# Kernel tuning notes

Measured on AMD Instinct MI355X. Metric: run time of the kernel, lower is better.

Reference implementation:

```python
import jax, jax.numpy as jnp
import numpy as np

S = 512      # num_seg (queries)
T = 16384    # frames
D = 512      # d_model
DFF = 2048   # dim_feedforward
EPS = 1e-5


def layer_norm(x, g, b):
    mu = jnp.mean(x, axis=-1, keepdims=True)
    var = jnp.mean((x - mu) ** 2, axis=-1, keepdims=True)
    return (x - mu) * jax.lax.rsqrt(var + EPS) * g + b


def setup_inputs() -> dict:
    key = jax.random.key(0)
    ks = jax.random.split(key, 16)
    inv = 1.0 / np.sqrt(D)
    invf = 1.0 / np.sqrt(DFF)
    # action_idx: exactly S contiguous segments over T frames
    action_idx = (jnp.arange(T, dtype=jnp.int32) * S) // T
    return {
        "tgt": jax.random.normal(ks[0], (S, 1, D), jnp.float32),
        "memory": jax.random.normal(ks[1], (T, 1, D), jnp.float32),
        "pos": jax.random.normal(ks[2], (T, 1, D), jnp.float32),
        "query_pos": jax.random.normal(ks[3], (S, 1, D), jnp.float32),
        "action_idx": action_idx,
        "W_tgt2": jax.random.uniform(ks[4], (D, D), jnp.float32, -inv, inv),
        "b_tgt2": jax.random.uniform(ks[5], (D,), jnp.float32, -inv, inv),
        "W1": jax.random.uniform(ks[6], (DFF, D), jnp.float32, -inv, inv),
        "b1": jax.random.uniform(ks[7], (DFF,), jnp.float32, -inv, inv),
        "W2": jax.random.uniform(ks[8], (D, DFF), jnp.float32, -invf, invf),
        "b2": jax.random.uniform(ks[9], (D,), jnp.float32, -invf, invf),
        "g2": jnp.ones((D,), jnp.float32),
        "be2": jnp.zeros((D,), jnp.float32),
        "g3": jnp.ones((D,), jnp.float32),
        "be3": jnp.zeros((D,), jnp.float32),
    }


def reference(tgt, memory, pos, query_pos, action_idx,
              W_tgt2, b_tgt2, W1, b1, W2, b2, g2, be2, g3, be3):
    num_seg, _, dim = tgt.shape
    q = tgt + query_pos          # [S, 1, D]
    k = memory + pos             # [T, 1, D]
    v = memory                   # [T, 1, D]

    # segment-neighbor mask: seg_id per frame; query s attends to frames in
    # segments {s-1, s, s+1}
    change = jnp.concatenate([jnp.zeros((1,), jnp.int32),
                              (action_idx[1:] != action_idx[:-1]).astype(jnp.int32)])
    seg_id = jnp.cumsum(change)                                   # [T]
    mask = jnp.abs(seg_id[None, :] - jnp.arange(num_seg)[:, None]) <= 1  # [S, T]

    scores = jnp.einsum("sbd,tbd->bst", q, k) / np.sqrt(dim)      # [1, S, T]
    scores = jnp.where(mask[None], scores, -jnp.inf)
    attn = jax.nn.softmax(scores, axis=-1)                        # [1, S, T]

    ctx = jnp.einsum("bst,tbd->sbd", attn, v)                     # [S, 1, D]
    tgt2 = jax.nn.relu(ctx) @ W_tgt2.T + b_tgt2                   # [S, 1, D]
    x = layer_norm(tgt + tgt2, g2, be2)
    ffn = jax.nn.relu(x @ W1.T + b1) @ W2.T + b2
    out = layer_norm(x + ffn, g3, be3)
    return out
```

## Files before the change

### kernel.cpp

```cpp
#include <hip/hip_runtime.h>
#include <math.h>

#define S_Q  512
#define T_F  16384
#define D_M  512
#define DFF_ 2048
#define SEG  32
#define SCALE 0.04419417382415922f

typedef __attribute__((ext_vector_type(8))) short short8;
typedef __attribute__((ext_vector_type(4))) float floatx4;

__device__ __forceinline__ unsigned short f2bf(float f) {
    unsigned int u = __builtin_bit_cast(unsigned int, f);
    u += 0x7FFFu + ((u >> 16) & 1u);
    return (unsigned short)(u >> 16);
}

__device__ __forceinline__ void async_copy16(const void* g, void* l) {
    __builtin_amdgcn_global_load_lds(
        (const __attribute__((address_space(1))) void*)g,
        (__attribute__((address_space(3))) void*)l, 16, 0, 0);
}

__global__ __launch_bounds__(256) void conv3_bf16(
    const float* __restrict__ w0, unsigned short* __restrict__ o0, int n0,
    const float* __restrict__ w1, unsigned short* __restrict__ o1, int n1,
    const float* __restrict__ w2, unsigned short* __restrict__ o2)
{
    int i = (blockIdx.x * 256 + threadIdx.x) * 4;
    const float* src; unsigned short* dst;
    if (i < n0)            { src = w0; dst = o0; }
    else if (i < n0 + n1)  { src = w1; dst = o1; i -= n0; }
    else                   { src = w2; dst = o2; i -= n0 + n1; }
    const float4 v = *(const float4*)(src + i);
    unsigned short o[4] = {f2bf(v.x), f2bf(v.y), f2bf(v.z), f2bf(v.w)};
    *(uint2*)(dst + i) = *(const uint2*)o;
}

__global__ __launch_bounds__(256) void attn_seg(
    const float* __restrict__ tgt, const float* __restrict__ memory,
    const float* __restrict__ pos, const float* __restrict__ qp,
    float* __restrict__ part,
    float2* __restrict__ me)
{
    const int j    = blockIdx.x;
    const int tid  = threadIdx.x;
    const int lane = tid & 63;
    const int wave = tid >> 6;

    __shared__ float v[SEG * D_M];
    __shared__ float sc[3][SEG];
    __shared__ float pr[3][SEG];

    {
        const float* g = memory + (size_t)j * SEG * D_M + (size_t)wave * 16 * 256 + lane * 4;
        #pragma unroll
        for (int r = 0; r < 16; ++r)
            async_copy16(g + r * 256, v + (wave * 16 + r) * 256);
    }

    float q0[8] = {}, q1[8] = {}, q2[8] = {};
    {
        const int d = lane * 8;
        if (j > 0) {
            const float4 a0 = *(const float4*)(tgt + (size_t)(j - 1) * D_M + d);
            const float4 a1 = *(const float4*)(tgt + (size_t)(j - 1) * D_M + d + 4);
            const float4 b0 = *(const float4*)(qp  + (size_t)(j - 1) * D_M + d);
            const float4 b1 = *(const float4*)(qp  + (size_t)(j - 1) * D_M + d + 4);
            q0[0]=a0.x+b0.x; q0[1]=a0.y+b0.y; q0[2]=a0.z+b0.z; q0[3]=a0.w+b0.w;
            q0[4]=a1.x+b1.x; q0[5]=a1.y+b1.y; q0[6]=a1.z+b1.z; q0[7]=a1.w+b1.w;
        }
        {
            const float4 a0 = *(const float4*)(tgt + (size_t)j * D_M + d);
            const float4 a1 = *(const float4*)(tgt + (size_t)j * D_M + d + 4);
            const float4 b0 = *(const float4*)(qp  + (size_t)j * D_M + d);
            const float4 b1 = *(const float4*)(qp  + (size_t)j * D_M + d + 4);
            q1[0]=a0.x+b0.x; q1[1]=a0.y+b0.y; q1[2]=a0.z+b0.z; q1[3]=a0.w+b0.w;
            q1[4]=a1.x+b1.x; q1[5]=a1.y+b1.y; q1[6]=a1.z+b1.z; q1[7]=a1.w+b1.w;
        }
        if (j < S_Q - 1) {
            const float4 a0 = *(const float4*)(tgt + (size_t)(j + 1) * D_M + d);
            const float4 a1 = *(const float4*)(tgt + (size_t)(j + 1) * D_M + d + 4);
            const float4 b0 = *(const float4*)(qp  + (size_t)(j + 1) * D_M + d);
            const float4 b1 = *(const float4*)(qp  + (size_t)(j + 1) * D_M + d + 4);
            q2[0]=a0.x+b0.x; q2[1]=a0.y+b0.y; q2[2]=a0.z+b0.z; q2[3]=a0.w+b0.w;
            q2[4]=a1.x+b1.x; q2[5]=a1.y+b1.y; q2[6]=a1.z+b1.z; q2[7]=a1.w+b1.w;
        }
    }
    __syncthreads();

    #pragma unroll
    for (int r = 0; r < 8; ++r) {
        const int f = wave * 8 + r;
        const size_t t = (size_t)(j * SEG + f);
        const float4 pA = *(const float4*)(pos + t * D_M + lane * 8);
        const float4 pB = *(const float4*)(pos + t * D_M + lane * 8 + 4);
        const float4 mA = *(const float4*)(v + f * D_M + lane * 8);
        const float4 mB = *(const float4*)(v + f * D_M + lane * 8 + 4);
        const float k8[8] = {mA.x+pA.x, mA.y+pA.y, mA.z+pA.z, mA.w+pA.w,
                             mB.x+pB.x, mB.y+pB.y, mB.z+pB.z, mB.w+pB.w};
        float a0 = 0.f, a1 = 0.f, a2 = 0.f;
        #pragma unroll
        for (int i = 0; i < 8; ++i) {
            a0 += k8[i] * q0[i]; a1 += k8[i] * q1[i]; a2 += k8[i] * q2[i];
        }
        #pragma unroll
        for (int off = 32; off > 0; off >>= 1) {
            a0 += __shfl_xor(a0, off, 64);
            a1 += __shfl_xor(a1, off, 64);
            a2 += __shfl_xor(a2, off, 64);
        }
        if (lane == 0) { sc[0][f] = a0 * SCALE; sc[1][f] = a1 * SCALE; sc[2][f] = a2 * SCALE; }
    }
    __syncthreads();

    if (wave < 3) {
        float mx = -1e30f;
        for (int f = 0; f < SEG; ++f) mx = fmaxf(mx, sc[wave][f]);
        float e = 0.f;
        for (int f = 0; f < SEG; ++f) {
            const float pe = __expf(sc[wave][f] - mx);
            e += pe;
            if (lane == 0) pr[wave][f] = pe;
        }
        const int q = j - 1 + wave;
        if (lane == 0 && q >= 0 && q < S_Q)
            me[q * 3 + (2 - wave)] = make_float2(mx, e);
    }
    __syncthreads();

    const int d0 = tid * 2;
    float c0x=0,c0y=0,c1x=0,c1y=0,c2x=0,c2y=0;
    for (int f = 0; f < SEG; ++f) {
        const float2 vv = *(const float2*)(v + f * D_M + d0);
        const float w0 = pr[0][f], w1 = pr[1][f], w2 = pr[2][f];
        c0x += w0 * vv.x; c0y += w0 * vv.y;
        c1x += w1 * vv.x; c1y += w1 * vv.y;
        c2x += w2 * vv.x; c2y += w2 * vv.y;
    }
    if (j > 0)
        *(float2*)(part + ((size_t)(j - 1) * 3 + 2) * D_M + d0) = make_float2(c0x, c0y);
    *(float2*)(part + ((size_t)j * 3 + 1) * D_M + d0) = make_float2(c1x, c1y);
    if (j < S_Q - 1)
        *(float2*)(part + ((size_t)(j + 1) * 3 + 0) * D_M + d0) = make_float2(c2x, c2y);
}

__global__ __launch_bounds__(256) void attn_merge(
    const float* __restrict__ part, const float2* __restrict__ me,
    unsigned short* __restrict__ rc)
{
    const int row  = blockIdx.x * 4 + (threadIdx.x >> 6);
    const int lane = threadIdx.x & 63;
    const int slo = (row == 0)       ? 1 : 0;
    const int shi = (row == S_Q - 1) ? 1 : 2;

    float mx = -1e30f;
    for (int s = slo; s <= shi; ++s) mx = fmaxf(mx, me[row * 3 + s].x);
    float den = 0.f, c[3] = {0.f, 0.f, 0.f};
    for (int s = slo; s <= shi; ++s) {
        c[s] = __expf(me[row * 3 + s].x - mx);
        den += me[row * 3 + s].y * c[s];
    }
    const float inv = 1.f / den;

    const int d = lane * 8;
    float acc[8] = {};
    for (int s = slo; s <= shi; ++s) {
        const float4 a = *(const float4*)(part + ((size_t)row * 3 + s) * D_M + d);
        const float4 b = *(const float4*)(part + ((size_t)row * 3 + s) * D_M + d + 4);
        acc[0]+=c[s]*a.x; acc[1]+=c[s]*a.y; acc[2]+=c[s]*a.z; acc[3]+=c[s]*a.w;
        acc[4]+=c[s]*b.x; acc[5]+=c[s]*b.y; acc[6]+=c[s]*b.z; acc[7]+=c[s]*b.w;
    }
    unsigned short o[8];
    #pragma unroll
    for (int i = 0; i < 8; ++i) o[i] = f2bf(fmaxf(acc[i] * inv, 0.f));
    *(uint4*)(rc + (size_t)row * D_M + d) = *(const uint4*)o;
}

template<int BM, int KSPLIT, bool RELU, bool ADDRES, bool OUT_BF16>
__global__ __launch_bounds__(256) void gemm_mfma(
    const unsigned short* __restrict__ A, const unsigned short* __restrict__ B,
    const float* __restrict__ bias, const float* __restrict__ res,
    void* __restrict__ Cout, int M, int N, int K)
{
    constexpr int BK = 64;
    constexpr int WT = BM / 2;
    constexpr int NT = WT / 16;
    constexpr int NR = BM / 32;
    __shared__ short As[2][BM * BK];
    __shared__ short Bs[2][BM * BK];

    const int tid  = threadIdx.x;
    const int lane = tid & 63;
    const int wave = tid >> 6;
    const int m0 = blockIdx.y * BM;
    const int n0 = blockIdx.x * BM;
    const int kbase = (K / KSPLIT) * blockIdx.z;
    const int niter = (K / KSPLIT) / BK;

    const int srow = tid >> 3;
    const int scol = (tid & 7) * 8;
    const int quad = lane >> 4;
    const int r16  = lane & 15;
    const int wm = (wave >> 1) * WT;
    const int wn = (wave & 1) * WT;

    floatx4 acc[NT][NT] = {};

    #pragma unroll
    for (int r = 0; r < NR; ++r) {
        async_copy16(A + (size_t)(m0 + r * 32 + srow) * K + kbase + scol, &As[0][r * 2048 + wave * 512]);
        async_copy16(B + (size_t)(n0 + r * 32 + srow) * K + kbase + scol, &Bs[0][r * 2048 + wave * 512]);
    }

    for (int it = 0; it < niter; ++it) {
        __syncthreads();
        if (it + 1 < niter) {
            const int k0 = kbase + (it + 1) * BK;
            const int nb = (it + 1) & 1;
            #pragma unroll
            for (int r = 0; r < NR; ++r) {
                async_copy16(A + (size_t)(m0 + r * 32 + srow) * K + k0 + scol, &As[nb][r * 2048 + wave * 512]);
                async_copy16(B + (size_t)(n0 + r * 32 + srow) * K + k0 + scol, &Bs[nb][r * 2048 + wave * 512]);
            }
        }
        const short* Ab = As[it & 1];
        const short* Bb = Bs[it & 1];
        #pragma unroll
        for (int ks = 0; ks < 2; ++ks) {
            short8 a[NT], bb[NT];
            #pragma unroll
            for (int i = 0; i < NT; ++i) {
                a[i]  = *(const short8*)(Ab + (wm + i * 16 + r16) * BK + ks * 32 + quad * 8);
                bb[i] = *(const short8*)(Bb + (wn + i * 16 + r16) * BK + ks * 32 + quad * 8);
            }
            #pragma unroll
            for (int i = 0; i < NT; ++i)
                #pragma unroll
                for (int jn = 0; jn < NT; ++jn)
                    acc[i][jn] = __builtin_amdgcn_mfma_f32_16x16x32_bf16(a[i], bb[jn], acc[i][jn], 0, 0, 0);
        }
    }

    #pragma unroll
    for (int nj = 0; nj < NT; ++nj) {
        const int col = n0 + wn + nj * 16 + r16;
        #pragma unroll
        for (int mi = 0; mi < NT; ++mi) {
            #pragma unroll
            for (int r = 0; r < 4; ++r) {
                const int row = m0 + wm + mi * 16 + quad * 4 + r;
                float cv = acc[mi][nj][r];
                if (KSPLIT > 1) {
                    ((float*)Cout)[((size_t)blockIdx.z * M + row) * N + col] = cv;
                } else {
                    cv += bias[col];
                    if (RELU)   cv = fmaxf(cv, 0.f);
                    if (ADDRES) cv += res[(size_t)row * N + col];
                    if (OUT_BF16)
                        ((unsigned short*)Cout)[(size_t)row * N + col] = f2bf(cv);
                    else
                        ((float*)Cout)[(size_t)row * N + col] = cv;
                }
            }
        }
    }
}

template<int NP, bool WRITE_BF16>
__global__ __launch_bounds__(256) void ln_merge(
    const float* __restrict__ parts,
    const float* __restrict__ res, const float* __restrict__ bias,
    const float* __restrict__ g, const float* __restrict__ be,
    float* __restrict__ out, unsigned short* __restrict__ out_bf)
{
    const int row  = blockIdx.x * 4 + (threadIdx.x >> 6);
    const int lane = threadIdx.x & 63;

    float vv[8];
    #pragma unroll
    for (int hh = 0; hh < 2; ++hh) {
        const int d = lane * 8 + hh * 4;
        float4 a = *(const float4*)(res + (size_t)row * D_M + d);
        const float4 b = *(const float4*)(bias + d);
        a.x += b.x; a.y += b.y; a.z += b.z; a.w += b.w;
        #pragma unroll
        for (int z = 0; z < NP; ++z) {
            const float4 p = *(const float4*)(parts + ((size_t)z * S_Q + row) * D_M + d);
            a.x += p.x; a.y += p.y; a.z += p.z; a.w += p.w;
        }
        vv[hh * 4 + 0] = a.x; vv[hh * 4 + 1] = a.y;
        vv[hh * 4 + 2] = a.z; vv[hh * 4 + 3] = a.w;
    }

    float sum = 0.f;
    #pragma unroll
    for (int i = 0; i < 8; ++i) sum += vv[i];
    #pragma unroll
    for (int off = 32; off > 0; off >>= 1) sum += __shfl_xor(sum, off, 64);
    const float mu = sum * (1.0f / 512.0f);

    float var = 0.f;
    #pragma unroll
    for (int i = 0; i < 8; ++i) { const float dd = vv[i] - mu; var += dd * dd; }
    #pragma unroll
    for (int off = 32; off > 0; off >>= 1) var += __shfl_xor(var, off, 64);
    const float rr = rsqrtf(var * (1.0f / 512.0f) + 1e-5f);

    #pragma unroll
    for (int hh = 0; hh < 2; ++hh) {
        const int d = lane * 8 + hh * 4;
        const float4 gg = *(const float4*)(g + d);
        const float4 bb = *(const float4*)(be + d);
        float4 o;
        o.x = (vv[hh*4+0] - mu) * rr * gg.x + bb.x;
        o.y = (vv[hh*4+1] - mu) * rr * gg.y + bb.y;
        o.z = (vv[hh*4+2] - mu) * rr * gg.z + bb.z;
        o.w = (vv[hh*4+3] - mu) * rr * gg.w + bb.w;
        *(float4*)(out + (size_t)row * D_M + d) = o;
        if (WRITE_BF16) {
            unsigned short ob[4] = {f2bf(o.x), f2bf(o.y), f2bf(o.z), f2bf(o.w)};
            *(uint2*)(out_bf + (size_t)row * D_M + d) = *(const uint2*)ob;
        }
    }
}

extern "C" void kernel_launch(void* const* d_in, const int* in_sizes, int n_in,
                              void* d_out, int out_size, void* d_ws, size_t ws_size,
                              hipStream_t stream) {
    const float* tgt       = (const float*)d_in[0];
    const float* memory    = (const float*)d_in[1];
    const float* pos       = (const float*)d_in[2];
    const float* query_pos = (const float*)d_in[3];
    const float* W_tgt2 = (const float*)d_in[5];
    const float* b_tgt2 = (const float*)d_in[6];
    const float* W1     = (const float*)d_in[7];
    const float* b1     = (const float*)d_in[8];
    const float* W2     = (const float*)d_in[9];
    const float* b2     = (const float*)d_in[10];
    const float* g2     = (const float*)d_in[11];
    const float* be2    = (const float*)d_in[12];
    const float* g3     = (const float*)d_in[13];
    const float* be3    = (const float*)d_in[14];
    float* out = (float*)d_out;

    char* w = (char*)d_ws;
    float* part   = (float*)w;
    float* gpart1 = (float*)(w + 3145728);
    float* gpart3 = (float*)w;
    size_t off = 5242880;
    float2* me          = (float2*)(w + off);          off += 12288;
    unsigned short* rc  = (unsigned short*)(w + off);  off += 524288;
    float* x            = (float*)(w + off);           off += 1048576;
    unsigned short* xb  = (unsigned short*)(w + off);  off += 524288;
    unsigned short* h   = (unsigned short*)(w + off);  off += 2097152;
    unsigned short* Wt2b= (unsigned short*)(w + off);  off += 524288;
    unsigned short* W1b = (unsigned short*)(w + off);  off += 2097152;
    unsigned short* W2b = (unsigned short*)(w + off);  off += 2097152;

    conv3_bf16<<<(D_M * D_M + DFF_ * D_M + D_M * DFF_) / 1024, 256, 0, stream>>>(
        W_tgt2, Wt2b, D_M * D_M, W1, W1b, DFF_ * D_M, W2, W2b);

    attn_seg<<<S_Q, 256, 0, stream>>>(tgt, memory, pos, query_pos, part, me);
    attn_merge<<<S_Q / 4, 256, 0, stream>>>(part, me, rc);

    gemm_mfma<32, 2, false, false, false><<<dim3(16, 16, 2), 256, 0, stream>>>(
        rc, Wt2b, nullptr, nullptr, gpart1, S_Q, D_M, D_M);
    ln_merge<2, true><<<S_Q / 4, 256, 0, stream>>>(
        gpart1, tgt, b_tgt2, g2, be2, x, xb);
    gemm_mfma<64, 1, true, false, true><<<dim3(DFF_ / 64, S_Q / 64, 1), 256, 0, stream>>>(
        xb, W1b, b1, nullptr, h, S_Q, DFF_, D_M);
    gemm_mfma<32, 4, false, false, false><<<dim3(16, 16, 4), 256, 0, stream>>>(
        h, W2b, nullptr, nullptr, gpart3, S_Q, D_M, DFF_);
    ln_merge<4, false><<<S_Q / 4, 256, 0, stream>>>(
        gpart3, x, b2, g3, be3, out, nullptr);
}
```

Baseline: 163.2 us.

## Fuse all stages into one cooperative persistent kernel with grid syncs

Replaces the eight separate launches with a single cooperative kernel of 512 blocks that runs attention, weight conversion, merge, the three GEMMs and both layer norms as phases separated by grid.sync(). The attention phase now reads memory directly from global instead of staging it in LDS, and every GEMM is re-tiled to 32x32 tiles with one MFMA accumulator per wave. The aim is to remove launch gaps and tail effects between small kernels. In exchange it adds grid-wide barrier cost, gives the FFN GEMMs smaller tiles with less reuse, and keeps a multi-kernel fallback in case the cooperative launch fails.

```diff
diff --git a/kernel.cpp b/kernel.cpp
--- a/kernel.cpp
+++ b/kernel.cpp
@@ -1,5 +1,8 @@
 #include <hip/hip_runtime.h>
+#include <hip/hip_cooperative_groups.h>
 #include <math.h>
+
+namespace cg = cooperative_groups;
 
 #define S_Q  512
 #define T_F  16384
@@ -23,81 +26,63 @@
         (__attribute__((address_space(3))) void*)l, 16, 0, 0);
 }
 
-__global__ __launch_bounds__(256) void conv3_bf16(
-    const float* __restrict__ w0, unsigned short* __restrict__ o0, int n0,
-    const float* __restrict__ w1, unsigned short* __restrict__ o1, int n1,
-    const float* __restrict__ w2, unsigned short* __restrict__ o2)
-{
-    int i = (blockIdx.x * 256 + threadIdx.x) * 4;
-    const float* src; unsigned short* dst;
-    if (i < n0)            { src = w0; dst = o0; }
-    else if (i < n0 + n1)  { src = w1; dst = o1; i -= n0; }
-    else                   { src = w2; dst = o2; i -= n0 + n1; }
-    const float4 v = *(const float4*)(src + i);
-    unsigned short o[4] = {f2bf(v.x), f2bf(v.y), f2bf(v.z), f2bf(v.w)};
-    *(uint2*)(dst + i) = *(const uint2*)o;
-}
-
-__global__ __launch_bounds__(256) void attn_seg(
-    const float* __restrict__ tgt, const float* __restrict__ memory,
-    const float* __restrict__ pos, const float* __restrict__ qp,
-    float* __restrict__ part,
-    float2* __restrict__ me)
-{
-    const int j    = blockIdx.x;
-    const int tid  = threadIdx.x;
-    const int lane = tid & 63;
-    const int wave = tid >> 6;
-
-    __shared__ float v[SEG * D_M];
-    __shared__ float sc[3][SEG];
-    __shared__ float pr[3][SEG];
-
-    {
-        const float* g = memory + (size_t)j * SEG * D_M + (size_t)wave * 16 * 256 + lane * 4;
-        #pragma unroll
-        for (int r = 0; r < 16; ++r)
-            async_copy16(g + r * 256, v + (wave * 16 + r) * 256);
-    }
+struct GSm { short A[2][2048]; short B[2][2048]; };
+struct ATm { float sc[3][SEG]; float pr[3][SEG]; };
+
+struct Params {
+    const float *tgt, *memory, *pos, *qp;
+    const float *b_tgt2, *b1, *b2, *g2, *be2, *g3, *be3;
+    const float *W_tgt2, *W1, *W2;
+    float *out;
+    float *part; float2 *me;
+    unsigned short *rc;
+    float *gpart1, *x;
+    unsigned short *xb, *h;
+    float *gpart3;
+    unsigned short *Wt2b, *W1b, *W2b;
+};
+
+__device__ __forceinline__ void attn_phase(const Params& p, int j, ATm* at)
+{
+    const int tid = threadIdx.x, lane = tid & 63, wave = tid >> 6;
 
     float q0[8] = {}, q1[8] = {}, q2[8] = {};
     {
         const int d = lane * 8;
         if (j > 0) {
-            const float4 a0 = *(const float4*)(tgt + (size_t)(j - 1) * D_M + d);
-            const float4 a1 = *(const float4*)(tgt + (size_t)(j - 1) * D_M + d + 4);
-            const float4 b0 = *(const float4*)(qp  + (size_t)(j - 1) * D_M + d);
-            const float4 b1 = *(const float4*)(qp  + (size_t)(j - 1) * D_M + d + 4);
+            const float4 a0 = *(const float4*)(p.tgt + (size_t)(j - 1) * D_M + d);
+            const float4 a1 = *(const float4*)(p.tgt + (size_t)(j - 1) * D_M + d + 4);
+            const float4 b0 = *(const float4*)(p.qp  + (size_t)(j - 1) * D_M + d);
+            const float4 b1 = *(const float4*)(p.qp  + (size_t)(j - 1) * D_M + d + 4);
             q0[0]=a0.x+b0.x; q0[1]=a0.y+b0.y; q0[2]=a0.z+b0.z; q0[3]=a0.w+b0.w;
             q0[4]=a1.x+b1.x; q0[5]=a1.y+b1.y; q0[6]=a1.z+b1.z; q0[7]=a1.w+b1.w;
         }
         {
-            const float4 a0 = *(const float4*)(tgt + (size_t)j * D_M + d);
-            const float4 a1 = *(const float4*)(tgt + (size_t)j * D_M + d + 4);
-            const float4 b0 = *(const float4*)(qp  + (size_t)j * D_M + d);
-            const float4 b1 = *(const float4*)(qp  + (size_t)j * D_M + d + 4);
+            const float4 a0 = *(const float4*)(p.tgt + (size_t)j * D_M + d);
+            const float4 a1 = *(const float4*)(p.tgt + (size_t)j * D_M + d + 4);
+            const float4 b0 = *(const float4*)(p.qp  + (size_t)j * D_M + d);
+            const float4 b1 = *(const float4*)(p.qp  + (size_t)j * D_M + d + 4);
             q1[0]=a0.x+b0.x; q1[1]=a0.y+b0.y; q1[2]=a0.z+b0.z; q1[3]=a0.w+b0.w;
             q1[4]=a1.x+b1.x; q1[5]=a1.y+b1.y; q1[6]=a1.z+b1.z; q1[7]=a1.w+b1.w;
         }
         if (j < S_Q - 1) {
-            const float4 a0 = *(const float4*)(tgt + (size_t)(j + 1) * D_M + d);
-            const float4 a1 = *(const float4*)(tgt + (size_t)(j + 1) * D_M + d + 4);
-            const float4 b0 = *(const float4*)(qp  + (size_t)(j + 1) * D_M + d);
-            const float4 b1 = *(const float4*)(qp  + (size_t)(j + 1) * D_M + d + 4);
+            const float4 a0 = *(const float4*)(p.tgt + (size_t)(j + 1) * D_M + d);
+            const float4 a1 = *(const float4*)(p.tgt + (size_t)(j + 1) * D_M + d + 4);
+            const float4 b0 = *(const float4*)(p.qp  + (size_t)(j + 1) * D_M + d);
+            const float4 b1 = *(const float4*)(p.qp  + (size_t)(j + 1) * D_M + d + 4);
             q2[0]=a0.x+b0.x; q2[1]=a0.y+b0.y; q2[2]=a0.z+b0.z; q2[3]=a0.w+b0.w;
             q2[4]=a1.x+b1.x; q2[5]=a1.y+b1.y; q2[6]=a1.z+b1.z; q2[7]=a1.w+b1.w;
         }
     }
-    __syncthreads();
 
     #pragma unroll
     for (int r = 0; r < 8; ++r) {
         const int f = wave * 8 + r;
         const size_t t = (size_t)(j * SEG + f);
-        const float4 pA = *(const float4*)(pos + t * D_M + lane * 8);
-        const float4 pB = *(const float4*)(pos + t * D_M + lane * 8 + 4);
-        const float4 mA = *(const float4*)(v + f * D_M + lane * 8);
-        const float4 mB = *(const float4*)(v + f * D_M + lane * 8 + 4);
+        const float4 mA = *(const float4*)(p.memory + t * D_M + lane * 8);
+        const float4 mB = *(const float4*)(p.memory + t * D_M + lane * 8 + 4);
+        const float4 pA = *(const float4*)(p.pos    + t * D_M + lane * 8);
+        const float4 pB = *(const float4*)(p.pos    + t * D_M + lane * 8 + 4);
         const float k8[8] = {mA.x+pA.x, mA.y+pA.y, mA.z+pA.z, mA.w+pA.w,
                              mB.x+pB.x, mB.y+pB.y, mB.z+pB.z, mB.w+pB.w};
         float a0 = 0.f, a1 = 0.f, a2 = 0.f;
@@ -111,171 +96,145 @@
             a1 += __shfl_xor(a1, off, 64);
             a2 += __shfl_xor(a2, off, 64);
         }
-        if (lane == 0) { sc[0][f] = a0 * SCALE; sc[1][f] = a1 * SCALE; sc[2][f] = a2 * SCALE; }
+        if (lane == 0) {
+            at->sc[0][f] = a0 * SCALE;
+            at->sc[1][f] = a1 * SCALE;
+            at->sc[2][f] = a2 * SCALE;
+        }
     }
     __syncthreads();
 
     if (wave < 3) {
         float mx = -1e30f;
-        for (int f = 0; f < SEG; ++f) mx = fmaxf(mx, sc[wave][f]);
+        for (int f = 0; f < SEG; ++f) mx = fmaxf(mx, at->sc[wave][f]);
         float e = 0.f;
         for (int f = 0; f < SEG; ++f) {
-            const float pe = __expf(sc[wave][f] - mx);
+            const float pe = __expf(at->sc[wave][f] - mx);
             e += pe;
-            if (lane == 0) pr[wave][f] = pe;
+            if (lane == 0) at->pr[wave][f] = pe;
         }
         const int q = j - 1 + wave;
         if (lane == 0 && q >= 0 && q < S_Q)
-            me[q * 3 + (2 - wave)] = make_float2(mx, e);
+            p.me[q * 3 + (2 - wave)] = make_float2(mx, e);
     }
     __syncthreads();
 
     const int d0 = tid * 2;
     float c0x=0,c0y=0,c1x=0,c1y=0,c2x=0,c2y=0;
     for (int f = 0; f < SEG; ++f) {
-        const float2 vv = *(const float2*)(v + f * D_M + d0);
-        const float w0 = pr[0][f], w1 = pr[1][f], w2 = pr[2][f];
+        const float2 vv = *(const float2*)(p.memory + (size_t)(j * SEG + f) * D_M + d0);
+        const float w0 = at->pr[0][f], w1 = at->pr[1][f], w2 = at->pr[2][f];
         c0x += w0 * vv.x; c0y += w0 * vv.y;
         c1x += w1 * vv.x; c1y += w1 * vv.y;
         c2x += w2 * vv.x; c2y += w2 * vv.y;
     }
     if (j > 0)
-        *(float2*)(part + ((size_t)(j - 1) * 3 + 2) * D_M + d0) = make_float2(c0x, c0y);
-    *(float2*)(part + ((size_t)j * 3 + 1) * D_M + d0) = make_float2(c1x, c1y);
+        *(float2*)(p.part + ((size_t)(j - 1) * 3 + 2) * D_M + d0) = make_float2(c0x, c0y);
+    *(float2*)(p.part + ((size_t)j * 3 + 1) * D_M + d0) = make_float2(c1x, c1y);
     if (j < S_Q - 1)
-        *(float2*)(part + ((size_t)(j + 1) * 3 + 0) * D_M + d0) = make_float2(c2x, c2y);
-}
-
-__global__ __launch_bounds__(256) void attn_merge(
-    const float* __restrict__ part, const float2* __restrict__ me,
-    unsigned short* __restrict__ rc)
-{
-    const int row  = blockIdx.x * 4 + (threadIdx.x >> 6);
-    const int lane = threadIdx.x & 63;
+        *(float2*)(p.part + ((size_t)(j + 1) * 3 + 0) * D_M + d0) = make_float2(c2x, c2y);
+}
+
+__device__ __forceinline__ void conv_phase(const Params& p, int i4)
+{
+    constexpr int n0 = D_M * D_M, n1 = DFF_ * D_M;
+    int i = i4 * 4;
+    const float* src; unsigned short* dst;
+    if (i < n0)            { src = p.W_tgt2; dst = p.Wt2b; }
+    else if (i < n0 + n1)  { src = p.W1;     dst = p.W1b;  i -= n0; }
+    else                   { src = p.W2;     dst = p.W2b;  i -= n0 + n1; }
+    const float4 vv = *(const float4*)(src + i);
+    unsigned short o[4] = {f2bf(vv.x), f2bf(vv.y), f2bf(vv.z), f2bf(vv.w)};
+    *(uint2*)(dst + i) = *(const uint2*)o;
+}
+
+__device__ __forceinline__ void merge_phase(const Params& p, int row)
+{
+    const int tid = threadIdx.x;
     const int slo = (row == 0)       ? 1 : 0;
     const int shi = (row == S_Q - 1) ? 1 : 2;
-
     float mx = -1e30f;
-    for (int s = slo; s <= shi; ++s) mx = fmaxf(mx, me[row * 3 + s].x);
+    for (int s = slo; s <= shi; ++s) mx = fmaxf(mx, p.me[row * 3 + s].x);
     float den = 0.f, c[3] = {0.f, 0.f, 0.f};
     for (int s = slo; s <= shi; ++s) {
-        c[s] = __expf(me[row * 3 + s].x - mx);
-        den += me[row * 3 + s].y * c[s];
+        c[s] = __expf(p.me[row * 3 + s].x - mx);
+        den += p.me[row * 3 + s].y * c[s];
     }
     const float inv = 1.f / den;
-
-    const int d = lane * 8;
-    float acc[8] = {};
+    const int d0 = tid * 2;
+    float ax = 0.f, ay = 0.f;
     for (int s = slo; s <= shi; ++s) {
-        const float4 a = *(const float4*)(part + ((size_t)row * 3 + s) * D_M + d);
-        const float4 b = *(const float4*)(part + ((size_t)row * 3 + s) * D_M + d + 4);
-        acc[0]+=c[s]*a.x; acc[1]+=c[s]*a.y; acc[2]+=c[s]*a.z; acc[3]+=c[s]*a.w;
-        acc[4]+=c[s]*b.x; acc[5]+=c[s]*b.y; acc[6]+=c[s]*b.z; acc[7]+=c[s]*b.w;
-    }
-    unsigned short o[8];
-    #pragma unroll
-    for (int i = 0; i < 8; ++i) o[i] = f2bf(fmaxf(acc[i] * inv, 0.f));
-    *(uint4*)(rc + (size_t)row * D_M + d) = *(const uint4*)o;
-}
-
-template<int BM, int KSPLIT, bool RELU, bool ADDRES, bool OUT_BF16>
-__global__ __launch_bounds__(256) void gemm_mfma(
-    const unsigned short* __restrict__ A, const unsigned short* __restrict__ B,
-    const float* __restrict__ bias, const float* __restrict__ res,
-    void* __restrict__ Cout, int M, int N, int K)
-{
-    constexpr int BK = 64;
-    constexpr int WT = BM / 2;
-    constexpr int NT = WT / 16;
-    constexpr int NR = BM / 32;
-    __shared__ short As[2][BM * BK];
-    __shared__ short Bs[2][BM * BK];
-
+        const float2 pp = *(const float2*)(p.part + ((size_t)row * 3 + s) * D_M + d0);
+        ax += c[s] * pp.x; ay += c[s] * pp.y;
+    }
+    const unsigned short o0 = f2bf(fmaxf(ax * inv, 0.f));
+    const unsigned short o1 = f2bf(fmaxf(ay * inv, 0.f));
+    *(unsigned int*)(p.rc + (size_t)row * D_M + d0) =
+        (unsigned int)o0 | ((unsigned int)o1 << 16);
+}
+
+template<bool PARTIAL>
+__device__ __forceinline__ void gemm_tile32(
+    GSm* sg, const unsigned short* __restrict__ A, const unsigned short* __restrict__ B,
+    int Nout, int K, int m0, int n0, int kbase, int niter,
+    const float* __restrict__ bias, void* __restrict__ Cout, int zoff)
+{
     const int tid  = threadIdx.x;
     const int lane = tid & 63;
     const int wave = tid >> 6;
-    const int m0 = blockIdx.y * BM;
-    const int n0 = blockIdx.x * BM;
-    const int kbase = (K / KSPLIT) * blockIdx.z;
-    const int niter = (K / KSPLIT) / BK;
-
     const int srow = tid >> 3;
     const int scol = (tid & 7) * 8;
     const int quad = lane >> 4;
     const int r16  = lane & 15;
-    const int wm = (wave >> 1) * WT;
-    const int wn = (wave & 1) * WT;
-
-    floatx4 acc[NT][NT] = {};
-
-    #pragma unroll
-    for (int r = 0; r < NR; ++r) {
-        async_copy16(A + (size_t)(m0 + r * 32 + srow) * K + kbase + scol, &As[0][r * 2048 + wave * 512]);
-        async_copy16(B + (size_t)(n0 + r * 32 + srow) * K + kbase + scol, &Bs[0][r * 2048 + wave * 512]);
-    }
+    const int wm = (wave >> 1) * 16;
+    const int wn = (wave & 1) * 16;
+
+    floatx4 acc = {0.f, 0.f, 0.f, 0.f};
+
+    async_copy16(A + (size_t)(m0 + srow) * K + kbase + scol, &sg->A[0][wave * 512]);
+    async_copy16(B + (size_t)(n0 + srow) * K + kbase + scol, &sg->B[0][wave * 512]);
 
     for (int it = 0; it < niter; ++it) {
         __syncthreads();
         if (it + 1 < niter) {
-            const int k0 = kbase + (it + 1) * BK;
+            const int k0 = kbase + (it + 1) * 64;
             const int nb = (it + 1) & 1;
-            #pragma unroll
-            for (int r = 0; r < NR; ++r) {
-                async_copy16(A + (size_t)(m0 + r * 32 + srow) * K + k0 + scol, &As[nb][r * 2048 + wave * 512]);
-                async_copy16(B + (size_t)(n0 + r * 32 + srow) * K + k0 + scol, &Bs[nb][r * 2048 + wave * 512]);
-            }
-        }
-        const short* Ab = As[it & 1];
-        const short* Bb = Bs[it & 1];
+            async_copy16(A + (size_t)(m0 + srow) * K + k0 + scol, &sg->A[nb][wave * 512]);
+            async_copy16(B + (size_t)(n0 + srow) * K + k0 + scol, &sg->B[nb][wave * 512]);
+        }
+        const short* Ab = sg->A[it & 1];
+        const short* Bb = sg->B[it & 1];
         #pragma unroll
         for (int ks = 0; ks < 2; ++ks) {
-            short8 a[NT], bb[NT];
-            #pragma unroll
-            for (int i = 0; i < NT; ++i) {
-                a[i]  = *(const short8*)(Ab + (wm + i * 16 + r16) * BK + ks * 32 + quad * 8);
-                bb[i] = *(const short8*)(Bb + (wn + i * 16 + r16) * BK + ks * 32 + quad * 8);
-            }
-            #pragma unroll
-            for (int i = 0; i < NT; ++i)
-                #pragma unroll
-                for (int jn = 0; jn < NT; ++jn)
-                    acc[i][jn] = __builtin_amdgcn_mfma_f32_16x16x32_bf16(a[i], bb[jn], acc[i][jn], 0, 0, 0);
-        }
-    }
-
-    #pragma unroll
-    for (int nj = 0; nj < NT; ++nj) {
-        const int col = n0 + wn + nj * 16 + r16;
-        #pragma unroll
-        for (int mi = 0; mi < NT; ++mi) {
-            #pragma unroll
-            for (int r = 0; r < 4; ++r) {
-                const int row = m0 + wm + mi * 16 + quad * 4 + r;
-                float cv = acc[mi][nj][r];
-                if (KSPLIT > 1) {
-                    ((float*)Cout)[((size_t)blockIdx.z * M + row) * N + col] = cv;
-                } else {
-                    cv += bias[col];
-                    if (RELU)   cv = fmaxf(cv, 0.f);
-                    if (ADDRES) cv += res[(size_t)row * N + col];
-                    if (OUT_BF16)
-                        ((unsigned short*)Cout)[(size_t)row * N + col] = f2bf(cv);
-                    else
-                        ((float*)Cout)[(size_t)row * N + col] = cv;
-                }
-            }
-        }
-    }
-}
-
-template<int NP, bool WRITE_BF16>
-__global__ __launch_bounds__(256) void ln_merge(
-    const float* __restrict__ parts,
-    const float* __restrict__ res, const float* __restrict__ bias,
-    const float* __restrict__ g, const float* __restrict__ be,
-    float* __restrict__ out, unsigned short* __restrict__ out_bf)
-{
-    const int row  = blockIdx.x * 4 + (threadIdx.x >> 6);
+            const short8 a = *(const short8*)(Ab + (wm + r16) * 64 + ks * 32 + quad * 8);
+            const short8 b = *(const short8*)(Bb + (wn + r16) * 64 + ks * 32 + quad * 8);
+            acc = __builtin_amdgcn_mfma_f32_16x16x32_bf16(a, b, acc, 0, 0, 0);
+        }
+    }
+
+    const int col = n0 + wn + r16;
+    const float bs = PARTIAL ? 0.f : bias[col];
+    #pragma unroll
+    for (int r = 0; r < 4; ++r) {
+        const int row = m0 + wm + quad * 4 + r;
+        float cv = acc[r];
+        if (PARTIAL) {
+            ((float*)Cout)[((size_t)(zoff + row)) * Nout + col] = cv;
+        } else {
+            cv = fmaxf(cv + bs, 0.f);
+            ((unsigned short*)Cout)[(size_t)row * Nout + col] = f2bf(cv);
+        }
+    }
+}
+
+template<bool WRITE_BF16>
+__device__ __forceinline__ void ln_rows(
+    const float* __restrict__ parts, const float* __restrict__ res,
+    const float* __restrict__ bias, const float* __restrict__ g,
+    const float* __restrict__ be, float* __restrict__ out,
+    unsigned short* __restrict__ out_bf, int rowblk)
+{
+    const int row  = rowblk * 4 + (threadIdx.x >> 6);
     const int lane = threadIdx.x & 63;
 
     float vv[8];
@@ -286,9 +245,9 @@
         const float4 b = *(const float4*)(bias + d);
         a.x += b.x; a.y += b.y; a.z += b.z; a.w += b.w;
         #pragma unroll
-        for (int z = 0; z < NP; ++z) {
-            const float4 p = *(const float4*)(parts + ((size_t)z * S_Q + row) * D_M + d);
-            a.x += p.x; a.y += p.y; a.z += p.z; a.w += p.w;
+        for (int z = 0; z < 2; ++z) {
+            const float4 pp = *(const float4*)(parts + ((size_t)z * S_Q + row) * D_M + d);
+            a.x += pp.x; a.y += pp.y; a.z += pp.z; a.w += pp.w;
         }
         vv[hh * 4 + 0] = a.x; vv[hh * 4 + 1] = a.y;
         vv[hh * 4 + 2] = a.z; vv[hh * 4 + 3] = a.w;
@@ -326,53 +285,137 @@
     }
 }
 
+__global__ __launch_bounds__(256, 2) void mega(Params p)
+{
+    __shared__ union { GSm g; ATm a; } sm;
+    cg::grid_group grid = cg::this_grid();
+    const int bid = blockIdx.x;
+    const int tid = threadIdx.x;
+
+    attn_phase(p, bid, &sm.a);
+    {
+        constexpr int tot4 = (D_M * D_M + DFF_ * D_M + D_M * DFF_) / 4;
+        for (int i4 = bid * 256 + tid; i4 < tot4; i4 += 512 * 256)
+            conv_phase(p, i4);
+    }
+    grid.sync();
+
+    merge_phase(p, bid);
+    grid.sync();
+
+    {
+        const int z = bid >> 8, by = (bid >> 4) & 15, bx = bid & 15;
+        gemm_tile32<true>(&sm.g, p.rc, p.Wt2b, D_M, D_M,
+                          by * 32, bx * 32, z * 256, 4, nullptr, p.gpart1, z * S_Q);
+    }
+    grid.sync();
+
+    if (bid < 128)
+        ln_rows<true>(p.gpart1, p.tgt, p.b_tgt2, p.g2, p.be2, p.x, p.xb, bid);
+    grid.sync();
+
+    #pragma unroll
+    for (int rep = 0; rep < 2; ++rep) {
+        const int t = bid + rep * 512;
+        gemm_tile32<false>(&sm.g, p.xb, p.W1b, DFF_, D_M,
+                           (t >> 6) * 32, (t & 63) * 32, 0, 8, p.b1, p.h, 0);
+    }
+    grid.sync();
+
+    {
+        const int z = bid >> 8, by = (bid >> 4) & 15, bx = bid & 15;
+        gemm_tile32<true>(&sm.g, p.h, p.W2b, D_M, DFF_,
+                          by * 32, bx * 32, z * 1024, 16, nullptr, p.gpart3, z * S_Q);
+    }
+    grid.sync();
+
+    if (bid < 128)
+        ln_rows<false>(p.gpart3, p.x, p.b2, p.g3, p.be3, p.out, nullptr, bid);
+}
+
+__global__ __launch_bounds__(256) void g_attn(Params p) {
+    __shared__ ATm at;
+    attn_phase(p, blockIdx.x, &at);
+}
+__global__ __launch_bounds__(256) void g_conv(Params p) {
+    conv_phase(p, blockIdx.x * 256 + threadIdx.x);
+}
+__global__ __launch_bounds__(256) void g_merge(Params p) {
+    merge_phase(p, blockIdx.x);
+}
+__global__ __launch_bounds__(256) void g_gemm1(Params p) {
+    __shared__ GSm sg;
+    const int b = blockIdx.x;
+    const int z = b >> 8, by = (b >> 4) & 15, bx = b & 15;
+    gemm_tile32<true>(&sg, p.rc, p.Wt2b, D_M, D_M,
+                      by * 32, bx * 32, z * 256, 4, nullptr, p.gpart1, z * S_Q);
+}
+__global__ __launch_bounds__(256) void g_ln1(Params p) {
+    ln_rows<true>(p.gpart1, p.tgt, p.b_tgt2, p.g2, p.be2, p.x, p.xb, blockIdx.x);
+}
+__global__ __launch_bounds__(256) void g_gemm2(Params p) {
+    __shared__ GSm sg;
+    const int t = blockIdx.x;
+    gemm_tile32<false>(&sg, p.xb, p.W1b, DFF_, D_M,
+                       (t >> 6) * 32, (t & 63) * 32, 0, 8, p.b1, p.h, 0);
+}
+__global__ __launch_bounds__(256) void g_gemm3(Params p) {
+    __shared__ GSm sg;
+    const int b = blockIdx.x;
+    const int z = b >> 8, by = (b >> 4) & 15, bx = b & 15;
+    gemm_tile32<true>(&sg, p.h, p.W2b, D_M, DFF_,
+                      by * 32, bx * 32, z * 1024, 16, nullptr, p.gpart3, z * S_Q);
+}
+__global__ __launch_bounds__(256) void g_ln2(Params p) {
+    ln_rows<false>(p.gpart3, p.x, p.b2, p.g3, p.be3, p.out, nullptr, blockIdx.x);
+}
+
 extern "C" void kernel_launch(void* const* d_in, const int* in_sizes, int n_in,
                               void* d_out, int out_size, void* d_ws, size_t ws_size,
                               hipStream_t stream) {
-    const float* tgt       = (const float*)d_in[0];
-    const float* memory    = (const float*)d_in[1];
-    const float* pos       = (const float*)d_in[2];
-    const float* query_pos = (const float*)d_in[3];
-    const float* W_tgt2 = (const float*)d_in[5];
-    const float* b_tgt2 = (const float*)d_in[6];
-    const float* W1     = (const float*)d_in[7];
-    const float* b1     = (const float*)d_in[8];
-    const float* W2     = (const float*)d_in[9];
-    const float* b2     = (const float*)d_in[10];
-    const float* g2     = (const float*)d_in[11];
-    const float* be2    = (const float*)d_in[12];
-    const float* g3     = (const float*)d_in[13];
-    const float* be3    = (const float*)d_in[14];
-    float* out = (float*)d_out;
+    Params p;
+    p.tgt    = (const float*)d_in[0];
+    p.memory = (const float*)d_in[1];
+    p.pos    = (const float*)d_in[2];
+    p.qp     = (const float*)d_in[3];
+    p.W_tgt2 = (const float*)d_in[5];
+    p.b_tgt2 = (const float*)d_in[6];
+    p.W1     = (const float*)d_in[7];
+    p.b1     = (const float*)d_in[8];
+    p.W2     = (const float*)d_in[9];
+    p.b2     = (const float*)d_in[10];
+    p.g2     = (const float*)d_in[11];
+    p.be2    = (const float*)d_in[12];
+    p.g3     = (const float*)d_in[13];
+    p.be3    = (const float*)d_in[14];
+    p.out    = (float*)d_out;
 
     char* w = (char*)d_ws;
-    float* part   = (float*)w;
-    float* gpart1 = (float*)(w + 3145728);
-    float* gpart3 = (float*)w;
-    size_t off = 5242880;
-    float2* me          = (float2*)(w + off);          off += 12288;
-    unsigned short* rc  = (unsigned short*)(w + off);  off += 524288;
-    float* x            = (float*)(w + off);           off += 1048576;
-    unsigned short* xb  = (unsigned short*)(w + off);  off += 524288;
-    unsigned short* h   = (unsigned short*)(w + off);  off += 2097152;
-    unsigned short* Wt2b= (unsigned short*)(w + off);  off += 524288;
-    unsigned short* W1b = (unsigned short*)(w + off);  off += 2097152;
-    unsigned short* W2b = (unsigned short*)(w + off);  off += 2097152;
-
-    conv3_bf16<<<(D_M * D_M + DFF_ * D_M + D_M * DFF_) / 1024, 256, 0, stream>>>(
-        W_tgt2, Wt2b, D_M * D_M, W1, W1b, DFF_ * D_M, W2, W2b);
-
-    attn_seg<<<S_Q, 256, 0, stream>>>(tgt, memory, pos, query_pos, part, me);
-    attn_merge<<<S_Q / 4, 256, 0, stream>>>(part, me, rc);
-
-    gemm_mfma<32, 2, false, false, false><<<dim3(16, 16, 2), 256, 0, stream>>>(
-        rc, Wt2b, nullptr, nullptr, gpart1, S_Q, D_M, D_M);
-    ln_merge<2, true><<<S_Q / 4, 256, 0, stream>>>(
-        gpart1, tgt, b_tgt2, g2, be2, x, xb);
-    gemm_mfma<64, 1, true, false, true><<<dim3(DFF_ / 64, S_Q / 64, 1), 256, 0, stream>>>(
-        xb, W1b, b1, nullptr, h, S_Q, DFF_, D_M);
-    gemm_mfma<32, 4, false, false, false><<<dim3(16, 16, 4), 256, 0, stream>>>(
-        h, W2b, nullptr, nullptr, gpart3, S_Q, D_M, DFF_);
-    ln_merge<4, false><<<S_Q / 4, 256, 0, stream>>>(
-        gpart3, x, b2, g3, be3, out, nullptr);
-}
+    size_t off = 0;
+    p.part   = (float*)(w + off);          off += (size_t)S_Q * 3 * D_M * 4;
+    p.me     = (float2*)(w + off);         off += (size_t)S_Q * 3 * 8;
+    p.rc     = (unsigned short*)(w + off); off += (size_t)S_Q * D_M * 2;
+    p.gpart1 = (float*)(w + off);          off += (size_t)2 * S_Q * D_M * 4;
+    p.x      = (float*)(w + off);          off += (size_t)S_Q * D_M * 4;
+    p.xb     = (unsigned short*)(w + off); off += (size_t)S_Q * D_M * 2;
+    p.h      = (unsigned short*)(w + off); off += (size_t)S_Q * DFF_ * 2;
+    p.gpart3 = (float*)(w + off);          off += (size_t)2 * S_Q * D_M * 4;
+    p.Wt2b   = (unsigned short*)(w + off); off += (size_t)D_M * D_M * 2;
+    p.W1b    = (unsigned short*)(w + off); off += (size_t)DFF_ * D_M * 2;
+    p.W2b    = (unsigned short*)(w + off); off += (size_t)D_M * DFF_ * 2;
+
+    void* args[] = { &p };
+    hipError_t err = hipLaunchCooperativeKernel(
+        (void*)mega, dim3(512), dim3(256), args, 0, stream);
+    if (err != hipSuccess) {
+        (void)hipGetLastError();
+        g_attn <<<S_Q, 256, 0, stream>>>(p);
+        g_conv <<<(D_M * D_M + DFF_ * D_M + D_M * DFF_) / 1024, 256, 0, stream>>>(p);
+        g_merge<<<S_Q, 256, 0, stream>>>(p);
+        g_gemm1<<<512, 256, 0, stream>>>(p);
+        g_ln1  <<<128, 256, 0, stream>>>(p);
+        g_gemm2<<<1024, 256, 0, stream>>>(p);
+        g_gemm3<<<512, 256, 0, stream>>>(p);
+        g_ln2  <<<128, 256, 0, stream>>>(p);
+    }
+}
```

Result: slower. 538.0 us (+229.6%).
